# Kernel optimization log

Measured on AMD Instinct MI355X. Metric: run time of the kernel, lower is better.

## Reference

```python
import jax, jax.numpy as jnp
import numpy as np

N = 50000
E = 1600000
B = 64
NODE_DIM = 12
EDGE_DIM = 4
HIDDEN = 128
HEADS = 4
C = HIDDEN // HEADS  # 32
LAYERS = 3
NEG_SLOPE = 0.2
EPS = 1e-16


def _ln(x, g, b):
    m = jnp.mean(x, -1, keepdims=True)
    v = jnp.mean((x - m) ** 2, -1, keepdims=True)
    return (x - m) * jax.lax.rsqrt(v + 1e-5) * g + b


def _gelu(x):
    return jax.nn.gelu(x, approximate=False)


def setup_inputs() -> dict:
    key = jax.random.key(0)
    ks = jax.random.split(key, 20)
    f = lambda k, sh: jax.random.normal(k, sh, jnp.float32) * 0.05
    return {
        "x": jax.random.normal(ks[0], (N, NODE_DIM), jnp.float32),
        "edge_attr": jax.random.normal(ks[1], (E, EDGE_DIM), jnp.float32),
        "edge_index": jax.random.randint(ks[2], (2, E), 0, N, jnp.int32),
        "batch": jnp.sort(jax.random.randint(ks[3], (N,), 0, B, jnp.int32)),
        "enc_w": f(ks[4], (NODE_DIM, HIDDEN)), "enc_b": jnp.zeros(HIDDEN, jnp.float32),
        "enc_g": jnp.ones(HIDDEN, jnp.float32), "enc_beta": jnp.zeros(HIDDEN, jnp.float32),
        "ee_w": f(ks[5], (EDGE_DIM, HIDDEN // 2)), "ee_b": jnp.zeros(HIDDEN // 2, jnp.float32),
        "gat_lin_w": f(ks[6], (LAYERS, HIDDEN, HEADS * C)),
        "gat_edge_w": f(ks[7], (LAYERS, HIDDEN // 2, HEADS * C)),
        "att_src": f(ks[8], (LAYERS, HEADS, C)),
        "att_dst": f(ks[9], (LAYERS, HEADS, C)),
        "att_edge": f(ks[10], (LAYERS, HEADS, C)),
        "gat_bias": jnp.zeros((LAYERS, HEADS * C), jnp.float32),
        "norm_g": jnp.ones((LAYERS, HIDDEN), jnp.float32),
        "norm_b": jnp.zeros((LAYERS, HIDDEN), jnp.float32),
        "freq_w1": f(ks[11], (2 * HIDDEN, HIDDEN)), "freq_b1": jnp.zeros(HIDDEN, jnp.float32),
        "freq_w2": f(ks[12], (HIDDEN, HIDDEN // 2)), "freq_b2": jnp.zeros(HIDDEN // 2, jnp.float32),
        "cls_w1": f(ks[13], (HIDDEN // 2, 64)), "cls_b1": jnp.zeros(64, jnp.float32),
        "cls_w2": f(ks[14], (64, 1)), "cls_b2": jnp.zeros(1, jnp.float32),
    }


def _forward(x, edge_attr, edge_index, batch,
             enc_w, enc_b, enc_g, enc_beta, ee_w, ee_b,
             gat_lin_w, gat_edge_w, att_src, att_dst, att_edge, gat_bias,
             norm_g, norm_b, freq_w1, freq_b1, freq_w2, freq_b2,
             cls_w1, cls_b1, cls_w2, cls_b2):
    n = x.shape[0]
    h = _gelu(_ln(x @ enc_w + enc_b, enc_g, enc_beta))          # [N, HIDDEN]
    ea = _gelu(edge_attr @ ee_w + ee_b)                          # [E, HIDDEN//2]
    src, dst = edge_index[0], edge_index[1]
    # add_self_loops with fill_value='mean': per-dst-node mean of incoming edge attrs
    deg = jax.ops.segment_sum(jnp.ones(src.shape, ea.dtype), dst, n)
    loop_attr = jax.ops.segment_sum(ea, dst, n) / jnp.maximum(deg, 1.0)[:, None]
    ar = jnp.arange(n, dtype=src.dtype)
    s_full = jnp.concatenate([src, ar])
    d_full = jnp.concatenate([dst, ar])
    ea_full = jnp.concatenate([ea, loop_attr], 0)                # [E+N, HIDDEN//2]
    for l in range(LAYERS):
        hh = (h @ gat_lin_w[l]).reshape(n, HEADS, C)             # [N, H, C]
        ef = (ea_full @ gat_edge_w[l]).reshape(-1, HEADS, C)     # [E+N, H, C]
        a_s = jnp.einsum('nhc,hc->nh', hh, att_src[l])
        a_d = jnp.einsum('nhc,hc->nh', hh, att_dst[l])
        alpha = a_s[s_full] + a_d[d_full] + jnp.einsum('ehc,hc->eh', ef, att_edge[l])
        alpha = jnp.where(alpha > 0, alpha, NEG_SLOPE * alpha)   # leaky_relu
        m = jax.ops.segment_max(alpha, d_full, n)                # segment softmax
        ex = jnp.exp(alpha - m[d_full])
        denom = jax.ops.segment_sum(ex, d_full, n)
        w = ex / (denom[d_full] + EPS)                           # [E+N, H]
        agg = jax.ops.segment_sum(w[:, :, None] * hh[s_full], d_full, n)
        agg = agg.reshape(n, HEADS * C) + gat_bias[l]
        h = _ln(h + agg, norm_g[l], norm_b[l])                   # residual + LayerNorm
    cnt = jax.ops.segment_sum(jnp.ones((n,), h.dtype), batch, B)
    mean = jax.ops.segment_sum(h, batch, B) / jnp.maximum(cnt, 1.0)[:, None]
    mx = jax.ops.segment_max(h, batch, B)
    mx = jnp.where(cnt[:, None] > 0, mx, 0.0)
    g = jnp.concatenate([mean, mx], -1)                          # [B, 2*HIDDEN]
    g = _gelu(_gelu(g @ freq_w1 + freq_b1) @ freq_w2 + freq_b2)
    logits = _gelu(g @ cls_w1 + cls_b1) @ cls_w2 + cls_b2
    return jax.nn.sigmoid(logits[:, 0])                          # [B]


def reference(x, edge_attr, edge_index, batch,
              enc_w, enc_b, enc_g, enc_beta, ee_w, ee_b,
              gat_lin_w, gat_edge_w, att_src, att_dst, att_edge, gat_bias,
              norm_g, norm_b, freq_w1, freq_b1, freq_w2, freq_b2,
              cls_w1, cls_b1, cls_w2, cls_b2):
    return _forward(x, edge_attr, edge_index, batch,
                    enc_w, enc_b, enc_g, enc_beta, ee_w, ee_b,
                    gat_lin_w, gat_edge_w, att_src, att_dst, att_edge, gat_bias,
                    norm_g, norm_b, freq_w1, freq_b1, freq_w2, freq_b2,
                    cls_w1, cls_b1, cls_w2, cls_b2)
```

## Files before the change

### kernel.cpp

```cpp
#include <hip/hip_runtime.h>
#include <float.h>
#include <math.h>

#define N_NODES 50000
#define N_EDGES 1600000
#define NB      64
#define HID     128
#define TOT     (N_EDGES + N_NODES)
#define PARTS   16
#define SCAN_NB 196
#define NPART4  4
#define PSIZE4  12500
#define SEPB    2048
#define GM_ROWS 64

typedef __attribute__((ext_vector_type(8))) short short8;
typedef __attribute__((ext_vector_type(4))) float f32x4;
typedef __attribute__((ext_vector_type(2))) float f32x2;

__device__ __forceinline__ float gelu_f(float x){
    return 0.5f * x * (1.0f + erff(x * 0.70710678118654752440f));
}

__device__ __forceinline__ float asf(unsigned int u){
    union { unsigned int i; float f; } c; c.i = u; return c.f;
}
__device__ __forceinline__ float bf2f(unsigned short u){
    return asf(((unsigned int)u) << 16);
}
__device__ __forceinline__ unsigned short f2bf(float x){
    union { float f; unsigned int i; } c; c.f = x;
    unsigned int r = c.i + 0x7fffu + ((c.i >> 16) & 1u);
    return (unsigned short)(r >> 16);
}
__device__ __forceinline__ uint2 pack4(float a, float b, float cc, float d){
    uint2 r;
    r.x = (unsigned int)f2bf(a) | ((unsigned int)f2bf(b) << 16);
    r.y = (unsigned int)f2bf(cc) | ((unsigned int)f2bf(d) << 16);
    return r;
}
__device__ __forceinline__ unsigned short sel_head(uint2 v, int hd){
    return (hd & 2) ? ((hd & 1) ? (unsigned short)(v.y >> 16) : (unsigned short)(v.y & 0xffff))
                    : ((hd & 1) ? (unsigned short)(v.x >> 16) : (unsigned short)(v.x & 0xffff));
}

__device__ __forceinline__ float blk_sum128(float v, float* red){
    #pragma unroll
    for (int m = 32; m > 0; m >>= 1) v += __shfl_xor(v, m, 64);
    __syncthreads();
    if ((threadIdx.x & 63) == 0) red[threadIdx.x >> 6] = v;
    __syncthreads();
    float r = red[0] + red[1];
    __syncthreads();
    return r;
}

__device__ __forceinline__ int blk_scan256(int v, int* wsum){
    int t = threadIdx.x, lane = t & 63, w = t >> 6;
    int x = v;
    #pragma unroll
    for (int off = 1; off < 64; off <<= 1){
        int y = __shfl_up(x, off, 64);
        if (lane >= off) x += y;
    }
    if (lane == 63) wsum[w] = x;
    __syncthreads();
    if (t == 0){
        int s = 0;
        #pragma unroll
        for (int i = 0; i < 4; i++){ int tmp = wsum[i]; wsum[i] = s; s += tmp; }
    }
    __syncthreads();
    return x + wsum[w];
}

__global__ void enc_kernel(const float* __restrict__ x, const float* __restrict__ enc_w,
                           const float* __restrict__ enc_b, const float* __restrict__ enc_g,
                           const float* __restrict__ enc_beta, float* __restrict__ h)
{
    __shared__ float xs[12];
    __shared__ float red[2];
    int n = blockIdx.x, t = threadIdx.x;
    if (t < 12) xs[t] = x[n * 12 + t];
    __syncthreads();
    float acc = enc_b[t];
    #pragma unroll
    for (int k = 0; k < 12; k++) acc += xs[k] * enc_w[k * HID + t];
    float mean = blk_sum128(acc, red) * (1.0f / HID);
    float d = acc - mean;
    float var = blk_sum128(d * d, red) * (1.0f / HID);
    float y = d * rsqrtf(var + 1e-5f) * enc_g[t] + enc_beta[t];
    h[(size_t)n * HID + t] = gelu_f(y);
}

__global__ void rank_kernel(const int* __restrict__ ei, int* __restrict__ row_count,
                            int* __restrict__ rank){
    int i = blockIdx.x * 256 + threadIdx.x;
    if (i < N_EDGES) rank[i] = atomicAdd(&row_count[ei[N_EDGES + i]], 1);
}

__global__ void scan1_kernel(const int* __restrict__ row_count, int* __restrict__ bsum){
    __shared__ int ws[4];
    int i = blockIdx.x * 256 + threadIdx.x;
    int v = (i < N_NODES) ? (row_count[i] + 1) : 0;
    int x = v;
    #pragma unroll
    for (int m = 32; m > 0; m >>= 1) x += __shfl_xor(x, m, 64);
    if ((threadIdx.x & 63) == 0) ws[threadIdx.x >> 6] = x;
    __syncthreads();
    if (threadIdx.x == 0) bsum[blockIdx.x] = ws[0] + ws[1] + ws[2] + ws[3];
}

__global__ void scan2_kernel(int* __restrict__ bsum){
    __shared__ int ws[4];
    int t = threadIdx.x;
    int v = (t < SCAN_NB) ? bsum[t] : 0;
    int incl = blk_scan256(v, ws);
    if (t < SCAN_NB) bsum[t] = incl - v;
}

__global__ void scan3_kernel(const int* __restrict__ row_count, const int* __restrict__ bsum,
                             int* __restrict__ row_ptr, int2* __restrict__ csr_se,
                             uint2* __restrict__ alp0, uint2* __restrict__ alp1,
                             uint2* __restrict__ alp2){
    __shared__ int ws[4];
    int i = blockIdx.x * 256 + threadIdx.x;
    int v = (i < N_NODES) ? (row_count[i] + 1) : 0;
    int incl = blk_scan256(v, ws) + bsum[blockIdx.x];
    if (i < N_NODES){
        row_ptr[i + 1] = incl;
        int sp = incl - 1;
        csr_se[sp] = make_int2(i, N_EDGES);
        uint2 z = make_uint2(0u, 0u);
        alp0[sp] = z; alp1[sp] = z; alp2[sp] = z;
    }
    if (i == 0) row_ptr[0] = 0;
}

__global__ void scatter_kernel(const int* __restrict__ ei, const int* __restrict__ rank,
                               const int* __restrict__ row_ptr, int2* __restrict__ csr_se){
    int part = blockIdx.x & (NPART4 - 1);
    int slice = blockIdx.x >> 2;
    int lo = part * PSIZE4, hi = lo + PSIZE4;
    int base = slice * SEPB;
    int iend = min(base + SEPB, N_EDGES);
    for (int i = base + threadIdx.x; i < iend; i += 256){
        int d = ei[N_EDGES + i];
        if (d < lo || d >= hi) continue;
        int pos = row_ptr[d] + rank[i];
        csr_se[pos] = make_int2(ei[i], i);
    }
}

__global__ void we3_kernel(const float* __restrict__ gat_edge_w, const float* __restrict__ att_edge,
                           float* __restrict__ We3)
{
    int t = threadIdx.x;
    int k = t >> 2, hd = t & 3;
    for (int l = 0; l < 3; l++){
        float s = 0.f;
        #pragma unroll
        for (int c = 0; c < 32; c++)
            s += gat_edge_w[(size_t)l * 64 * HID + k * HID + hd * 32 + c]
               * att_edge[l * HID + hd * 32 + c];
        We3[(l * 64 + k) * 4 + hd] = s;
    }
}

__global__ void ae_pos_kernel(const int2* __restrict__ csr_se, const float4* __restrict__ edge_attr,
                              const float* __restrict__ ee_w, const float* __restrict__ ee_b,
                              const float* __restrict__ We3,
                              uint2* __restrict__ alp0, uint2* __restrict__ alp1,
                              uint2* __restrict__ alp2)
{
    int p = blockIdx.x * 256 + threadIdx.x;
    if (p >= TOT) return;
    int2 se = csr_se[p];
    if (se.y >= N_EDGES) return;
    float4 ea = edge_attr[se.y];
    const f32x2* w0 = (const f32x2*)(ee_w);
    const f32x2* w1 = (const f32x2*)(ee_w + 64);
    const f32x2* w2 = (const f32x2*)(ee_w + 128);
    const f32x2* w3 = (const f32x2*)(ee_w + 192);
    const f32x2* bb = (const f32x2*)(ee_b);
    const f32x2* Wv = (const f32x2*)(We3);

    f32x2 eax = {ea.x, ea.x}, eay = {ea.y, ea.y}, eaz = {ea.z, ea.z}, eaw = {ea.w, ea.w};
    const f32x2 one2 = {1.0f, 1.0f};
    const f32x2 c044 = {0.044715f, 0.044715f};
    const f32x2 kneg = {-2.3021182f, -2.3021182f};

    f32x2 acc[6];
    #pragma unroll
    for (int i = 0; i < 6; i++) acc[i] = (f32x2){0.f, 0.f};

    #pragma unroll 4
    for (int m = 0; m < 32; m++){
        f32x2 u = bb[m];
        u = __builtin_elementwise_fma(eax, w0[m], u);
        u = __builtin_elementwise_fma(eay, w1[m], u);
        u = __builtin_elementwise_fma(eaz, w2[m], u);
        u = __builtin_elementwise_fma(eaw, w3[m], u);
        f32x2 a = u * u;
        f32x2 b = __builtin_elementwise_fma(c044, a, one2);
        f32x2 c = u * kneg;
        f32x2 z = c * b;
        f32x2 e = { __builtin_amdgcn_exp2f(z.x), __builtin_amdgcn_exp2f(z.y) };
        f32x2 d = e + one2;
        f32x2 r = { __builtin_amdgcn_rcpf(d.x), __builtin_amdgcn_rcpf(d.y) };
        f32x2 g = u * r;
        f32x2 gx = {g.x, g.x}, gy = {g.y, g.y};
        #pragma unroll
        for (int l = 0; l < 3; l++){
            int base = (l * 64 + 2 * m) * 2;
            acc[l*2+0] = __builtin_elementwise_fma(gx, Wv[base + 0], acc[l*2+0]);
            acc[l*2+1] = __builtin_elementwise_fma(gx, Wv[base + 1], acc[l*2+1]);
            acc[l*2+0] = __builtin_elementwise_fma(gy, Wv[base + 2], acc[l*2+0]);
            acc[l*2+1] = __builtin_elementwise_fma(gy, Wv[base + 3], acc[l*2+1]);
        }
    }
    alp0[p] = pack4(acc[0].x, acc[0].y, acc[1].x, acc[1].y);
    alp1[p] = pack4(acc[2].x, acc[2].y, acc[3].x, acc[3].y);
    alp2[p] = pack4(acc[4].x, acc[4].y, acc[5].x, acc[5].y);
}

__global__ __launch_bounds__(64) void selfae_kernel(
        const int* __restrict__ row_ptr,
        uint2* __restrict__ alp0, uint2* __restrict__ alp1, uint2* __restrict__ alp2)
{
    int n = blockIdx.x, t = threadIdx.x;
    int start = row_ptr[n], end = row_ptr[n + 1];
    int sp = end - 1;
    float v[12];
    #pragma unroll
    for (int i = 0; i < 12; i++) v[i] = 0.f;
    for (int p = start + t; p < end; p += 64){
        uint2 q0 = alp0[p], q1 = alp1[p], q2 = alp2[p];
        v[0] += asf(q0.x << 16); v[1] += asf(q0.x & 0xffff0000u);
        v[2] += asf(q0.y << 16); v[3] += asf(q0.y & 0xffff0000u);
        v[4] += asf(q1.x << 16); v[5] += asf(q1.x & 0xffff0000u);
        v[6] += asf(q1.y << 16); v[7] += asf(q1.y & 0xffff0000u);
        v[8] += asf(q2.x << 16); v[9] += asf(q2.x & 0xffff0000u);
        v[10] += asf(q2.y << 16); v[11] += asf(q2.y & 0xffff0000u);
    }
    #pragma unroll
    for (int m = 1; m < 64; m <<= 1){
        #pragma unroll
        for (int i = 0; i < 12; i++) v[i] += __shfl_xor(v[i], m, 64);
    }
    if (t == 0){
        float inv = 1.0f / (float)max(end - start - 1, 1);
        alp0[sp] = pack4(v[0]*inv, v[1]*inv, v[2]*inv,  v[3]*inv);
        alp1[sp] = pack4(v[4]*inv, v[5]*inv, v[6]*inv,  v[7]*inv);
        alp2[sp] = pack4(v[8]*inv, v[9]*inv, v[10]*inv, v[11]*inv);
    }
}

__global__ __launch_bounds__(256) void gemm_hh_kernel(
        const float* __restrict__ h, const float* __restrict__ W,
        const float* __restrict__ att_s, const float* __restrict__ att_d,
        unsigned char* __restrict__ hh8, float* __restrict__ a_s,
        float* __restrict__ a_d)
{
    __shared__ __align__(16) unsigned char smem[128 * 136 * 2];
    unsigned short* Wt = (unsigned short*)smem;
    float* Dsh = (float*)smem;
    int t = threadIdx.x;

    for (int i = t; i < 128 * 128; i += 256){
        int k = i >> 7, n = i & 127;
        Wt[n * 136 + k] = f2bf(W[i]);
    }
    __syncthreads();

    int wave = t >> 6, lane = t & 63;
    int mm = lane & 15, quad = lane >> 4;
    int row = blockIdx.x * GM_ROWS + wave * 16 + mm;
    int rclamp = min(row, N_NODES - 1);
    const float* hrow = h + (size_t)rclamp * HID;

    f32x4 acc[8];
    #pragma unroll
    for (int i = 0; i < 8; i++) acc[i] = (f32x4){0.f, 0.f, 0.f, 0.f};

    #pragma unroll
    for (int kc = 0; kc < 4; kc++){
        int k0 = kc * 32 + quad * 8;
        float4 a0 = *(const float4*)(hrow + k0);
        float4 a1 = *(const float4*)(hrow + k0 + 4);
        short8 af;
        af[0] = (short)f2bf(a0.x); af[1] = (short)f2bf(a0.y);
        af[2] = (short)f2bf(a0.z); af[3] = (short)f2bf(a0.w);
        af[4] = (short)f2bf(a1.x); af[5] = (short)f2bf(a1.y);
        af[6] = (short)f2bf(a1.z); af[7] = (short)f2bf(a1.w);
        #pragma unroll
        for (int nt = 0; nt < 8; nt++){
            short8 bf = *(const short8*)&Wt[(nt * 16 + mm) * 136 + k0];
            acc[nt] = __builtin_amdgcn_mfma_f32_16x16x32_bf16(af, bf, acc[nt], 0, 0, 0);
        }
    }
    __syncthreads();

    #pragma unroll
    for (int nt = 0; nt < 8; nt++){
        #pragma unroll
        for (int r = 0; r < 4; r++){
            Dsh[(wave * 16 + quad * 4 + r) * 132 + nt * 16 + mm] = acc[nt][r];
        }
    }
    __syncthreads();

    int c = t & 127, rp = t >> 7;
    float as_w = att_s[c], ad_w = att_d[c];
    int head = c >> 5;
    for (int rr = rp; rr < GM_ROWS; rr += 2){
        int n = blockIdx.x * GM_ROWS + rr;
        if (n >= N_NODES) break;
        float val = Dsh[rr * 132 + c];
        unsigned int pk = (unsigned int)__builtin_amdgcn_cvt_pk_fp8_f32(val, 0.f, 0, false);
        hh8[(size_t)n * HID + c] = (unsigned char)(pk & 0xFFu);
        float vs = val * as_w, vd = val * ad_w;
        #pragma unroll
        for (int m2 = 16; m2 > 0; m2 >>= 1){
            vs += __shfl_xor(vs, m2, 32);
            vd += __shfl_xor(vd, m2, 32);
        }
        if ((c & 31) == 0){
            a_s[n * 4 + head] = vs;
            a_d[n * 4 + head] = vd;
        }
    }
}

__global__ __launch_bounds__(64) void agg_kernel(
        const float* __restrict__ a_s, const float* __restrict__ a_d,
        const int* __restrict__ row_ptr, const int2* __restrict__ csr_se,
        const uint2* __restrict__ alp, const uint2* __restrict__ hhv2,
        float* __restrict__ h, const float* __restrict__ gat_bias,
        const float* __restrict__ norm_g, const float* __restrict__ norm_b)
{
    int n = blockIdx.x, ln = threadIdx.x;
    int g = ln >> 4, l16 = ln & 15, hd = l16 >> 2;
    int start = row_ptr[n], end = row_ptr[n + 1];
    float ad_h = a_d[n * 4 + hd];

    f32x2 a01A = {0.f,0.f}, a23A = {0.f,0.f}, a45A = {0.f,0.f}, a67A = {0.f,0.f};
    f32x2 a01B = {0.f,0.f}, a23B = {0.f,0.f}, a45B = {0.f,0.f}, a67B = {0.f,0.f};
    float exA = 0.f, exB = 0.f;

    auto step = [&](int pp, f32x2& a01, f32x2& a23, f32x2& a45, f32x2& a67, float& es){
        int2 se = csr_se[pp];
        uint2 av = alp[pp];
        float ae = bf2f(sel_head(av, hd));
        float x0 = a_s[se.x * 4 + hd] + ad_h + ae;
        x0 = x0 > 0.f ? x0 : 0.2f * x0;
        float e0 = __expf(x0);
        es += e0;
        uint2 q = hhv2[(size_t)se.x * 16 + l16];
        f32x2 c01 = __builtin_amdgcn_cvt_pk_f32_fp8(q.x, false);
        f32x2 c23 = __builtin_amdgcn_cvt_pk_f32_fp8(q.x, true);
        f32x2 c45 = __builtin_amdgcn_cvt_pk_f32_fp8(q.y, false);
        f32x2 c67 = __builtin_amdgcn_cvt_pk_f32_fp8(q.y, true);
        f32x2 ee = {e0, e0};
        a01 = __builtin_elementwise_fma(ee, c01, a01);
        a23 = __builtin_elementwise_fma(ee, c23, a23);
        a45 = __builtin_elementwise_fma(ee, c45, a45);
        a67 = __builtin_elementwise_fma(ee, c67, a67);
    };

    int p = start + g;
    for (; p + 4 < end; p += 8){
        step(p,     a01A, a23A, a45A, a67A, exA);
        step(p + 4, a01B, a23B, a45B, a67B, exB);
    }
    if (p < end) step(p, a01A, a23A, a45A, a67A, exA);

    f32x2 a01 = a01A + a01B, a23 = a23A + a23B, a45 = a45A + a45B, a67 = a67A + a67B;
    float ex = exA + exB;
    #pragma unroll
    for (int m = 16; m <= 32; m <<= 1){
        a01.x += __shfl_xor(a01.x, m, 64); a01.y += __shfl_xor(a01.y, m, 64);
        a23.x += __shfl_xor(a23.x, m, 64); a23.y += __shfl_xor(a23.y, m, 64);
        a45.x += __shfl_xor(a45.x, m, 64); a45.y += __shfl_xor(a45.y, m, 64);
        a67.x += __shfl_xor(a67.x, m, 64); a67.y += __shfl_xor(a67.y, m, 64);
        ex += __shfl_xor(ex, m, 64);
    }
    float invd = 1.0f / (ex + 1e-16f);

    const float4* hrow4 = (const float4*)(h + (size_t)n * HID);
    float4 hv0 = hrow4[l16 * 2], hv1 = hrow4[l16 * 2 + 1];
    float4 b0 = ((const float4*)gat_bias)[l16 * 2];
    float4 b1 = ((const float4*)gat_bias)[l16 * 2 + 1];
    float y0 = hv0.x + a01.x * invd + b0.x;
    float y1 = hv0.y + a01.y * invd + b0.y;
    float y2 = hv0.z + a23.x * invd + b0.z;
    float y3 = hv0.w + a23.y * invd + b0.w;
    float y4 = hv1.x + a45.x * invd + b1.x;
    float y5 = hv1.y + a45.y * invd + b1.y;
    float y6 = hv1.z + a67.x * invd + b1.z;
    float y7 = hv1.w + a67.y * invd + b1.w;

    float s = y0 + y1 + y2 + y3 + y4 + y5 + y6 + y7;
    #pragma unroll
    for (int m = 1; m <= 8; m <<= 1) s += __shfl_xor(s, m, 64);
    float mean = s * (1.0f / HID);
    float d0 = y0 - mean, d1 = y1 - mean, d2 = y2 - mean, d3 = y3 - mean;
    float d4 = y4 - mean, d5 = y5 - mean, d6 = y6 - mean, d7 = y7 - mean;
    float vsum = d0*d0 + d1*d1 + d2*d2 + d3*d3 + d4*d4 + d5*d5 + d6*d6 + d7*d7;
    #pragma unroll
    for (int m = 1; m <= 8; m <<= 1) vsum += __shfl_xor(vsum, m, 64);
    float rstd = rsqrtf(vsum * (1.0f / HID) + 1e-5f);

    if (ln < 16){
        float4 g0 = ((const float4*)norm_g)[l16 * 2];
        float4 g1 = ((const float4*)norm_g)[l16 * 2 + 1];
        float4 nb0 = ((const float4*)norm_b)[l16 * 2];
        float4 nb1 = ((const float4*)norm_b)[l16 * 2 + 1];
        float4 r0 = make_float4(d0 * rstd * g0.x + nb0.x, d1 * rstd * g0.y + nb0.y,
                                d2 * rstd * g0.z + nb0.z, d3 * rstd * g0.w + nb0.w);
        float4 r1 = make_float4(d4 * rstd * g1.x + nb1.x, d5 * rstd * g1.y + nb1.y,
                                d6 * rstd * g1.z + nb1.z, d7 * rstd * g1.w + nb1.w);
        float4* orow = (float4*)(h + (size_t)n * HID);
        orow[l16 * 2] = r0;
        orow[l16 * 2 + 1] = r1;
    }
}

__global__ void bounds_kernel(const int* __restrict__ batch, int* __restrict__ bstart){
    int b = threadIdx.x;
    if (b > NB) return;
    int lo = 0, hi = N_NODES;
    while (lo < hi){
        int mid = (lo + hi) >> 1;
        if (batch[mid] < b) lo = mid + 1; else hi = mid;
    }
    bstart[b] = lo;
}

__global__ void pool_kernel(const float* __restrict__ h, const int* __restrict__ bstart,
                            float* __restrict__ psum, float* __restrict__ pmax){
    int b = blockIdx.x, part = blockIdx.y, t = threadIdx.x;
    int s = bstart[b], e = bstart[b + 1];
    int len = e - s;
    int chunk = (len + PARTS - 1) / PARTS;
    int cs = s + part * chunk;
    int ce = min(cs + chunk, e);
    float sum = 0.f, mx = -FLT_MAX;
    for (int n = cs; n < ce; ++n){
        float v = h[(size_t)n * HID + t];
        sum += v; mx = fmaxf(mx, v);
    }
    int slot = (b * PARTS + part) * HID + t;
    psum[slot] = sum;
    pmax[slot] = mx;
}

__global__ void mlp_kernel(const float* __restrict__ psum, const float* __restrict__ pmax,
                           const int* __restrict__ bstart,
                           const float* __restrict__ fw1, const float* __restrict__ fb1,
                           const float* __restrict__ fw2, const float* __restrict__ fb2,
                           const float* __restrict__ cw1, const float* __restrict__ cb1,
                           const float* __restrict__ cw2, const float* __restrict__ cb2,
                           float* __restrict__ out)
{
    __shared__ float g[256];
    __shared__ float y1[128];
    __shared__ float y2[64];
    __shared__ float y3[64];
    __shared__ float red[2];
    int b = blockIdx.x, t = threadIdx.x;
    float sum = 0.f, mx = -FLT_MAX;
    for (int p = 0; p < PARTS; p++){
        int slot = (b * PARTS + p) * HID + t;
        sum += psum[slot];
        mx = fmaxf(mx, pmax[slot]);
    }
    int cnt = bstart[b + 1] - bstart[b];
    float mean = sum / (float)max(cnt, 1);
    if (cnt <= 0) mx = 0.f;
    g[t] = mean; g[128 + t] = mx;
    __syncthreads();
    float a1 = fb1[t];
    for (int k = 0; k < 256; k++) a1 += g[k] * fw1[k * 128 + t];
    y1[t] = gelu_f(a1);
    __syncthreads();
    if (t < 64){
        float a2 = fb2[t];
        for (int k = 0; k < 128; k++) a2 += y1[k] * fw2[k * 64 + t];
        y2[t] = gelu_f(a2);
    }
    __syncthreads();
    if (t < 64){
        float a3 = cb1[t];
        for (int k = 0; k < 64; k++) a3 += y2[k] * cw1[k * 64 + t];
        y3[t] = gelu_f(a3);
    }
    __syncthreads();
    float v = (t < 64) ? y3[t] * cw2[t] : 0.f;
    float s = blk_sum128(v, red);
    if (t == 0){
        float logit = s + cb2[0];
        out[b] = 1.0f / (1.0f + expf(-logit));
    }
}

extern "C" void kernel_launch(void* const* d_in, const int* in_sizes, int n_in,
                              void* d_out, int out_size, void* d_ws, size_t ws_size,
                              hipStream_t stream)
{
    const float* x         = (const float*)d_in[0];
    const float* edge_attr = (const float*)d_in[1];
    const int*   edge_idx  = (const int*)  d_in[2];
    const int*   batch     = (const int*)  d_in[3];
    const float* enc_w     = (const float*)d_in[4];
    const float* enc_b     = (const float*)d_in[5];
    const float* enc_g     = (const float*)d_in[6];
    const float* enc_beta  = (const float*)d_in[7];
    const float* ee_w      = (const float*)d_in[8];
    const float* ee_b      = (const float*)d_in[9];
    const float* gat_lin_w = (const float*)d_in[10];
    const float* gat_edge_w= (const float*)d_in[11];
    const float* att_src   = (const float*)d_in[12];
    const float* att_dst   = (const float*)d_in[13];
    const float* att_edge  = (const float*)d_in[14];
    const float* gat_bias  = (const float*)d_in[15];
    const float* norm_g    = (const float*)d_in[16];
    const float* norm_b    = (const float*)d_in[17];
    const float* fw1       = (const float*)d_in[18];
    const float* fb1       = (const float*)d_in[19];
    const float* fw2       = (const float*)d_in[20];
    const float* fb2       = (const float*)d_in[21];
    const float* cw1       = (const float*)d_in[22];
    const float* cb1       = (const float*)d_in[23];
    const float* cw2       = (const float*)d_in[24];
    const float* cb2       = (const float*)d_in[25];
    float* out = (float*)d_out;

    char* wsp = (char*)d_ws;
    size_t off = 0;
    auto alloc = [&](size_t bytes) -> void* {
        void* p = wsp + off;
        off += (bytes + 255) & ~(size_t)255;
        return p;
    };
    float*          h        = (float*)alloc((size_t)N_NODES * HID * 4);
    unsigned char*  hh8      = (unsigned char*)alloc((size_t)N_NODES * HID);
    float*          a_s      = (float*)alloc((size_t)N_NODES * 4 * 4);
    float*          a_d      = (float*)alloc((size_t)N_NODES * 4 * 4);
    uint2*          alp0     = (uint2*)alloc((size_t)TOT * 8);
    uint2*          alp1     = (uint2*)alloc((size_t)TOT * 8);
    uint2*          alp2     = (uint2*)alloc((size_t)TOT * 8);
    int2*           csr_se   = (int2*) alloc((size_t)TOT * 8);
    int*            rank     = (int*)  alloc((size_t)N_EDGES * 4);
    int*            row_ptr  = (int*)  alloc((size_t)(N_NODES + 1) * 4);
    int*            row_count= (int*)  alloc((size_t)N_NODES * 4);
    int*            bsum     = (int*)  alloc((size_t)SCAN_NB * 4);
    float*          We3      = (float*)alloc(3 * 64 * 4 * 4);
    int*            bstart   = (int*)  alloc((NB + 1) * 4);
    float*          psum     = (float*)alloc((size_t)NB * PARTS * HID * 4);
    float*          pmax     = (float*)alloc((size_t)NB * PARTS * HID * 4);

    hipLaunchKernelGGL(enc_kernel, dim3(N_NODES), dim3(128), 0, stream,
                       x, enc_w, enc_b, enc_g, enc_beta, h);

    hipMemsetAsync(row_count, 0, (size_t)N_NODES * 4, stream);
    hipLaunchKernelGGL(rank_kernel, dim3((N_EDGES + 255) / 256), dim3(256), 0, stream,
                       edge_idx, row_count, rank);
    hipLaunchKernelGGL(scan1_kernel, dim3(SCAN_NB), dim3(256), 0, stream, row_count, bsum);
    hipLaunchKernelGGL(scan2_kernel, dim3(1), dim3(256), 0, stream, bsum);
    hipLaunchKernelGGL(scan3_kernel, dim3(SCAN_NB), dim3(256), 0, stream,
                       row_count, bsum, row_ptr, csr_se, alp0, alp1, alp2);
    {
        int slices_s = (N_EDGES + SEPB - 1) / SEPB;
        hipLaunchKernelGGL(scatter_kernel, dim3(slices_s * NPART4), dim3(256), 0, stream,
                           edge_idx, rank, row_ptr, csr_se);
    }

    hipLaunchKernelGGL(we3_kernel, dim3(1), dim3(256), 0, stream, gat_edge_w, att_edge, We3);
    hipLaunchKernelGGL(ae_pos_kernel, dim3((TOT + 255) / 256), dim3(256), 0, stream,
                       (const int2*)csr_se, (const float4*)edge_attr, ee_w, ee_b, We3,
                       alp0, alp1, alp2);
    hipLaunchKernelGGL(selfae_kernel, dim3(N_NODES), dim3(64), 0, stream,
                       row_ptr, alp0, alp1, alp2);

    uint2* alps[3] = {alp0, alp1, alp2};
    int gemm_blocks = (N_NODES + GM_ROWS - 1) / GM_ROWS;
    for (int l = 0; l < 3; l++){
        hipLaunchKernelGGL(gemm_hh_kernel, dim3(gemm_blocks), dim3(256), 0, stream,
                           h, gat_lin_w + (size_t)l * HID * HID,
                           att_src + (size_t)l * HID, att_dst + (size_t)l * HID,
                           hh8, a_s, a_d);
        hipLaunchKernelGGL(agg_kernel, dim3(N_NODES), dim3(64), 0, stream,
                           a_s, a_d, row_ptr, (const int2*)csr_se,
                           (const uint2*)alps[l], (const uint2*)hh8, h,
                           gat_bias + (size_t)l * HID, norm_g + (size_t)l * HID,
                           norm_b + (size_t)l * HID);
    }

    hipLaunchKernelGGL(bounds_kernel, dim3(1), dim3(128), 0, stream, batch, bstart);
    hipLaunchKernelGGL(pool_kernel, dim3(NB, PARTS), dim3(128), 0, stream, h, bstart, psum, pmax);
    hipLaunchKernelGGL(mlp_kernel, dim3(NB), dim3(128), 0, stream,
                       psum, pmax, bstart, fw1, fb1, fw2, fb2, cw1, cb1, cw2, cb2, out);
}
```

Baseline: 641.4 us.

## Build CSR with per-slice LDS histograms instead of global atomic ranks

Replaces the global-atomic rank computation and rank-based scatter with a two-pass counting sort. Edges are split into 64 slices and nodes into 8 ranges, and each block builds an LDS histogram. A column scan turns the per-slice counts into offsets, and a build kernel recomputes local ranks in LDS to place edges. This removes 1.6M contended global atomics and the rank array, at the cost of a 12.8MB histogram buffer and reading the edge list 8 times per pass.

```diff
diff --git a/kernel.cpp b/kernel.cpp
--- a/kernel.cpp
+++ b/kernel.cpp
@@ -9,9 +9,9 @@
 #define TOT     (N_EDGES + N_NODES)
 #define PARTS   16
 #define SCAN_NB 196
-#define NPART4  4
-#define PSIZE4  12500
-#define SEPB    2048
+#define NSLICE  64
+#define SLICE_E (N_EDGES / NSLICE)
+#define PRANGE  6250
 #define GM_ROWS 64
 
 typedef __attribute__((ext_vector_type(8))) short short8;
@@ -93,10 +93,34 @@
     h[(size_t)n * HID + t] = gelu_f(y);
 }
 
-__global__ void rank_kernel(const int* __restrict__ ei, int* __restrict__ row_count,
-                            int* __restrict__ rank){
-    int i = blockIdx.x * 256 + threadIdx.x;
-    if (i < N_EDGES) rank[i] = atomicAdd(&row_count[ei[N_EDGES + i]], 1);
+__global__ __launch_bounds__(256) void hist_kernel(const int* __restrict__ ei,
+                                                   int* __restrict__ hist){
+    __shared__ int lh[PRANGE];
+    int s = blockIdx.x >> 3, p = blockIdx.x & 7;
+    int lo = p * PRANGE;
+    for (int j = threadIdx.x; j < PRANGE; j += 256) lh[j] = 0;
+    __syncthreads();
+    int base = s * SLICE_E;
+    for (int i = base + threadIdx.x; i < base + SLICE_E; i += 256){
+        int d = ei[N_EDGES + i] - lo;
+        if ((unsigned)d < (unsigned)PRANGE) atomicAdd(&lh[d], 1);
+    }
+    __syncthreads();
+    int* hrow = hist + (size_t)s * N_NODES + lo;
+    for (int j = threadIdx.x; j < PRANGE; j += 256) hrow[j] = lh[j];
+}
+
+__global__ void colscan_kernel(int* __restrict__ hist, int* __restrict__ row_count){
+    int d = blockIdx.x * 256 + threadIdx.x;
+    if (d >= N_NODES) return;
+    int run = 0;
+    #pragma unroll 4
+    for (int s = 0; s < NSLICE; s++){
+        int v = hist[(size_t)s * N_NODES + d];
+        hist[(size_t)s * N_NODES + d] = run;
+        run += v;
+    }
+    row_count[d] = run;
 }
 
 __global__ void scan1_kernel(const int* __restrict__ row_count, int* __restrict__ bsum){
@@ -137,18 +161,25 @@
     if (i == 0) row_ptr[0] = 0;
 }
 
-__global__ void scatter_kernel(const int* __restrict__ ei, const int* __restrict__ rank,
-                               const int* __restrict__ row_ptr, int2* __restrict__ csr_se){
-    int part = blockIdx.x & (NPART4 - 1);
-    int slice = blockIdx.x >> 2;
-    int lo = part * PSIZE4, hi = lo + PSIZE4;
-    int base = slice * SEPB;
-    int iend = min(base + SEPB, N_EDGES);
-    for (int i = base + threadIdx.x; i < iend; i += 256){
+__global__ __launch_bounds__(256) void build_kernel(const int* __restrict__ ei,
+                                                    const int* __restrict__ hist,
+                                                    const int* __restrict__ row_ptr,
+                                                    int2* __restrict__ csr_se){
+    __shared__ int lh[PRANGE];
+    int s = blockIdx.x >> 3, p = blockIdx.x & 7;
+    int lo = p * PRANGE;
+    for (int j = threadIdx.x; j < PRANGE; j += 256) lh[j] = 0;
+    __syncthreads();
+    int base = s * SLICE_E;
+    const int* hrow = hist + (size_t)s * N_NODES;
+    for (int i = base + threadIdx.x; i < base + SLICE_E; i += 256){
         int d = ei[N_EDGES + i];
-        if (d < lo || d >= hi) continue;
-        int pos = row_ptr[d] + rank[i];
-        csr_se[pos] = make_int2(ei[i], i);
+        int dl = d - lo;
+        if ((unsigned)dl < (unsigned)PRANGE){
+            int local = atomicAdd(&lh[dl], 1);
+            int pos = row_ptr[d] + hrow[d] + local;
+            csr_se[pos] = make_int2(ei[i], i);
+        }
     }
 }
 
@@ -551,7 +582,7 @@
     uint2*          alp1     = (uint2*)alloc((size_t)TOT * 8);
     uint2*          alp2     = (uint2*)alloc((size_t)TOT * 8);
     int2*           csr_se   = (int2*) alloc((size_t)TOT * 8);
-    int*            rank     = (int*)  alloc((size_t)N_EDGES * 4);
+    int*            hist     = (int*)  alloc((size_t)NSLICE * N_NODES * 4);
     int*            row_ptr  = (int*)  alloc((size_t)(N_NODES + 1) * 4);
     int*            row_count= (int*)  alloc((size_t)N_NODES * 4);
     int*            bsum     = (int*)  alloc((size_t)SCAN_NB * 4);
@@ -563,18 +594,14 @@
     hipLaunchKernelGGL(enc_kernel, dim3(N_NODES), dim3(128), 0, stream,
                        x, enc_w, enc_b, enc_g, enc_beta, h);
 
-    hipMemsetAsync(row_count, 0, (size_t)N_NODES * 4, stream);
-    hipLaunchKernelGGL(rank_kernel, dim3((N_EDGES + 255) / 256), dim3(256), 0, stream,
-                       edge_idx, row_count, rank);
+    hipLaunchKernelGGL(hist_kernel, dim3(NSLICE * 8), dim3(256), 0, stream, edge_idx, hist);
+    hipLaunchKernelGGL(colscan_kernel, dim3(SCAN_NB), dim3(256), 0, stream, hist, row_count);
     hipLaunchKernelGGL(scan1_kernel, dim3(SCAN_NB), dim3(256), 0, stream, row_count, bsum);
     hipLaunchKernelGGL(scan2_kernel, dim3(1), dim3(256), 0, stream, bsum);
     hipLaunchKernelGGL(scan3_kernel, dim3(SCAN_NB), dim3(256), 0, stream,
                        row_count, bsum, row_ptr, csr_se, alp0, alp1, alp2);
-    {
-        int slices_s = (N_EDGES + SEPB - 1) / SEPB;
-        hipLaunchKernelGGL(scatter_kernel, dim3(slices_s * NPART4), dim3(256), 0, stream,
-                           edge_idx, rank, row_ptr, csr_se);
-    }
+    hipLaunchKernelGGL(build_kernel, dim3(NSLICE * 8), dim3(256), 0, stream,
+                       edge_idx, hist, row_ptr, csr_se);
 
     hipLaunchKernelGGL(we3_kernel, dim3(1), dim3(256), 0, stream, gat_edge_w, att_edge, We3);
     hipLaunchKernelGGL(ae_pos_kernel, dim3((TOT + 255) / 256), dim3(256), 0, stream,
```

After: 658.4 us. +2.7%, slower.
